# Performance work log

Measured on AMD Instinct MI355X. Metric: run time of the kernel, lower is better.

The kernel has to match this reference:

```python
import jax, jax.numpy as jnp
import numpy as np

DIM = 256
N = 8192

def setup_inputs() -> dict:
    key = jax.random.key(0)
    kx, kq, kk, kv = jax.random.split(key, 4)
    X = jax.random.normal(kx, (N, DIM), dtype=jnp.float32)
    # nn.Linear weights are [out, in]; xavier-uniform-like scale via normal/sqrt(dim)
    Wq = jax.random.normal(kq, (DIM, DIM), dtype=jnp.float32) / np.sqrt(DIM)
    Wk = jax.random.normal(kk, (DIM, DIM), dtype=jnp.float32) / np.sqrt(DIM)
    Wv = jax.random.normal(kv, (DIM, DIM), dtype=jnp.float32) / np.sqrt(DIM)
    return {"X": X, "Wq": Wq, "Wk": Wk, "Wv": Wv}

def reference(X, Wq, Wk, Wv):
    # nn.Linear(no bias): y = X @ W.T
    Q = X @ Wq.T  # [N, D]
    K = X @ Wk.T
    V = X @ Wv.T
    scores = (Q @ K.T) / jnp.sqrt(jnp.asarray(DIM, dtype=X.dtype))  # [N, N]
    softed = jax.nn.softmax(scores, axis=-1)
    return softed @ V  # [N, D]
```

## Files before the change

kernel.cpp:

```cpp
#include <hip/hip_runtime.h>
#include <math.h>

#define N 8192
#define D 256
#define QBLK 128
#define KBLK 32

typedef float f32x4 __attribute__((ext_vector_type(4)));
typedef float f32x16 __attribute__((ext_vector_type(16)));
typedef short bf16x8 __attribute__((ext_vector_type(8)));

#define MFMA16(a, b, c) __builtin_amdgcn_mfma_f32_16x16x32_bf16((a), (b), (c), 0, 0, 0)
#define MFMA32(a, b, c) __builtin_amdgcn_mfma_f32_32x32x16_bf16((a), (b), (c), 0, 0, 0)
#define BAR() __builtin_amdgcn_s_barrier()
#define CFENCE() asm volatile("" ::: "memory")

__device__ __forceinline__ unsigned short f2b(float f) {
    unsigned u = __builtin_bit_cast(unsigned, f);
    u = u + 0x7fffu + ((u >> 16) & 1u);
    return (unsigned short)(u >> 16);
}
__device__ __forceinline__ unsigned pk2(float a, float b) {
    return (unsigned)f2b(a) | ((unsigned)f2b(b) << 16);
}
__device__ __forceinline__ unsigned cvtpk(float a, float b) {
    unsigned r;
    asm("v_cvt_pk_bf16_f32 %0, %1, %2" : "=v"(r) : "v"(a), "v"(b));
    return r;
}
__device__ __forceinline__ float b2f(short s) {
    unsigned x = ((unsigned)(unsigned short)s) << 16;
    return __builtin_bit_cast(float, x);
}

__global__ __launch_bounds__(256) void proj_mfma(
    const float* __restrict__ X, const float* __restrict__ Wq,
    const float* __restrict__ Wk, const float* __restrict__ Wv,
    unsigned short* __restrict__ Qb, unsigned short* __restrict__ Kb,
    unsigned short* __restrict__ Vt)
{
    __shared__ char Wl[32768];
    const int z = blockIdx.z;
    const float* W = (z == 0) ? Wq : (z == 1) ? Wk : Wv;
    const int r0 = blockIdx.x * 64;
    const int c0 = blockIdx.y * 64;
    const int t = threadIdx.x, w = t >> 6, l = t & 63;
    const int lo = l & 15, hi = l >> 4;

    #pragma unroll
    for (int i = 0; i < 16; ++i) {
        int e4 = t + i * 256;
        int col = e4 >> 6, kk4 = e4 & 63;
        float4 f = *(const float4*)&W[(size_t)(c0 + col) * D + kk4 * 4];
        unsigned long long v = (unsigned long long)pk2(f.x, f.y)
                             | ((unsigned long long)pk2(f.z, f.w) << 32);
        *(unsigned long long*)(Wl + col * 512 + ((kk4 * 8) ^ ((col & 7) << 4))) = v;
    }
    __syncthreads();

    bf16x8 xf[8];
    {
        const float* xr = X + (size_t)(r0 + w * 16 + lo) * D;
        #pragma unroll
        for (int ks = 0; ks < 8; ++ks) {
            float4 a = *(const float4*)(xr + ks * 32 + hi * 8);
            float4 b = *(const float4*)(xr + ks * 32 + hi * 8 + 4);
            bf16x8 v;
            v[0] = (short)f2b(a.x); v[1] = (short)f2b(a.y);
            v[2] = (short)f2b(a.z); v[3] = (short)f2b(a.w);
            v[4] = (short)f2b(b.x); v[5] = (short)f2b(b.y);
            v[6] = (short)f2b(b.z); v[7] = (short)f2b(b.w);
            xf[ks] = v;
        }
    }

    f32x4 acc[4];
    #pragma unroll
    for (int nc = 0; nc < 4; ++nc) acc[nc] = (f32x4){0.f, 0.f, 0.f, 0.f};
    #pragma unroll
    for (int ks = 0; ks < 8; ++ks) {
        #pragma unroll
        for (int nc = 0; nc < 4; ++nc) {
            int col = nc * 16 + lo;
            bf16x8 wf = *(const bf16x8*)(Wl + col * 512 +
                                         ((ks * 64 + hi * 16) ^ ((col & 7) << 4)));
            acc[nc] = MFMA16(xf[ks], wf, acc[nc]);
        }
    }

    if (z < 2) {
        unsigned short* Y = z ? Kb : Qb;
        #pragma unroll
        for (int nc = 0; nc < 4; ++nc)
            #pragma unroll
            for (int r = 0; r < 4; ++r)
                Y[(size_t)(r0 + w * 16 + hi * 4 + r) * D + c0 + nc * 16 + lo] = f2b(acc[nc][r]);
    } else {
        #pragma unroll
        for (int nc = 0; nc < 4; ++nc) {
            unsigned long long v = (unsigned long long)pk2(acc[nc][0], acc[nc][1])
                                 | ((unsigned long long)pk2(acc[nc][2], acc[nc][3]) << 32);
            *(unsigned long long*)&Vt[(size_t)(c0 + nc * 16 + lo) * N + r0 + w * 16 + hi * 4] = v;
        }
    }
}

template <int KSPLIT>
__global__ __launch_bounds__(256, 2) void attn_mfma(
    const unsigned short* __restrict__ Qb,
    const unsigned short* __restrict__ Kb,
    const unsigned short* __restrict__ Vt,
    unsigned short* __restrict__ Opart,
    float2* __restrict__ ml)
{
    extern __shared__ char smem[];
    const int t = threadIdx.x;
    const int w = t >> 6;
    const int l = t & 63;
    const int r = l & 31;
    const int hi1 = l >> 5;
    const int bid = blockIdx.x;
    const int split = bid % KSPLIT;
    const int xblk = bid / KSPLIT;
    const int q0 = xblk * QBLK + w * 32;
    const int kbase = split * (N / KSPLIT);
    const int NTS = N / KSPLIT / KBLK;
    const int p0 = bid & (NTS - 1);

    unsigned ksoff[4], vsoff[4];
    #pragma unroll
    for (int i = 0; i < 4; ++i) {
        int c = t + i * 256;
        int rr = c >> 5, xc = c & 31;
        int pk = (rr & 0x13) | ((rr & 4) << 1) | ((rr & 8) >> 1);
        ksoff[i] = (unsigned)(pk * D + (xc ^ (rr & 7)) * 8);
        int dd = c >> 2, x2 = c & 3;
        vsoff[i] = (unsigned)(dd * N + (x2 ^ ((dd >> 1) & 3)) * 8);
    }

    auto stageK = [&](char* kbuf, int tile) {
        const unsigned koff = (unsigned)(kbase + tile * KBLK) * D;
        #pragma unroll
        for (int i = 0; i < 4; ++i)
            __builtin_amdgcn_global_load_lds(
                (const __attribute__((address_space(1))) void*)(Kb + koff + ksoff[i]),
                (__attribute__((address_space(3))) void*)(kbuf + (t + i * 256) * 16), 16, 0, 0);
    };
    auto stageV = [&](char* vbuf, int tile) {
        const unsigned voff = (unsigned)(kbase + tile * KBLK);
        #pragma unroll
        for (int i = 0; i < 4; ++i)
            __builtin_amdgcn_global_load_lds(
                (const __attribute__((address_space(1))) void*)(Vt + voff + vsoff[i]),
                (__attribute__((address_space(3))) void*)(vbuf + (t + i * 256) * 16), 16, 0, 0);
    };

    bf16x8 qf[16];
    {
        const unsigned short* qrow = Qb + (size_t)(q0 + r) * D;
        #pragma unroll
        for (int ks = 0; ks < 16; ++ks)
            qf[ks] = *(const bf16x8*)(qrow + ks * 16 + hi1 * 8);
    }

    stageK(smem, p0);
    stageV(smem + 32768, p0);
    stageK(smem + 16384, (p0 + 1) & (NTS - 1));
    stageV(smem + 32768 + 16384, (p0 + 1) & (NTS - 1));

    f32x16 Oacc[8];
    #pragma unroll
    for (int nc = 0; nc < 8; ++nc)
        #pragma unroll
        for (int e = 0; e < 16; ++e) Oacc[nc][e] = 0.f;
    float m_run = -INFINITY, l_run = 0.f;
    const float scale2 = 0.09016994f;

    for (int tt = 0; tt < NTS; ++tt) {
        const int cur = tt & 1;
        char* Kl = smem + cur * 16384;
        char* Vl = smem + 32768 + cur * 16384;

        if (tt + 1 == NTS) asm volatile("s_waitcnt vmcnt(0)" ::: "memory");
        else               asm volatile("s_waitcnt vmcnt(8)" ::: "memory");
        BAR(); CFENCE();

        f32x16 sacc;
        #pragma unroll
        for (int e = 0; e < 16; ++e) sacc[e] = 0.f;

        bf16x8 kf8[8];
        #pragma unroll
        for (int j = 0; j < 8; ++j)
            kf8[j] = *(const bf16x8*)(Kl + r * 512 + (((j * 2 + hi1) ^ (r & 7)) * 16));
        __builtin_amdgcn_s_setprio(1);
        #pragma unroll
        for (int j = 0; j < 8; ++j)
            sacc = MFMA32(kf8[j], qf[j], sacc);
        __builtin_amdgcn_s_setprio(0);

        bf16x8 kg8[8];
        #pragma unroll
        for (int j = 0; j < 8; ++j)
            kg8[j] = *(const bf16x8*)(Kl + r * 512 + ((((8 + j) * 2 + hi1) ^ (r & 7)) * 16));
        __builtin_amdgcn_s_setprio(1);
        #pragma unroll
        for (int j = 0; j < 8; ++j)
            sacc = MFMA32(kg8[j], qf[8 + j], sacc);
        __builtin_amdgcn_s_setprio(0);

        float m0 = fmaxf(fmaxf(sacc[0], sacc[1]),   fmaxf(sacc[2], sacc[3]));
        float m1 = fmaxf(fmaxf(sacc[4], sacc[5]),   fmaxf(sacc[6], sacc[7]));
        float m2 = fmaxf(fmaxf(sacc[8], sacc[9]),   fmaxf(sacc[10], sacc[11]));
        float m3 = fmaxf(fmaxf(sacc[12], sacc[13]), fmaxf(sacc[14], sacc[15]));
        float pm = fmaxf(fmaxf(m0, m1), fmaxf(m2, m3)) * scale2;

        bool need = pm > m_run + 11.0f;
        if (__builtin_expect(__any(need), 0)) {
            float m2x = fmaxf(pm, __shfl_xor(pm, 32));
            float m_new = fmaxf(m_run, m2x);
            float corr = exp2f(m_run - m_new);
            m_run = m_new;
            l_run *= corr;
            #pragma unroll
            for (int nc = 0; nc < 8; ++nc)
                #pragma unroll
                for (int e = 0; e < 16; ++e) Oacc[nc][e] *= corr;
        }

        bf16x8 pb[2];
        float sum = 0.f;
        #pragma unroll
        for (int s1 = 0; s1 < 2; ++s1) {
            union { unsigned u[4]; bf16x8 v; } uu;
            #pragma unroll
            for (int j2 = 0; j2 < 4; ++j2) {
                float a = __builtin_amdgcn_exp2f(sacc[s1 * 8 + j2 * 2]     * scale2 - m_run);
                float b = __builtin_amdgcn_exp2f(sacc[s1 * 8 + j2 * 2 + 1] * scale2 - m_run);
                sum += a + b;
                uu.u[j2] = cvtpk(a, b);
            }
            pb[s1] = uu.v;
        }

        bf16x8 vf8[8];
        #pragma unroll
        for (int nc = 0; nc < 4; ++nc) {
            const char* vrow = Vl + (nc * 32 + r) * 64;
            vf8[nc * 2 + 0] = *(const bf16x8*)(vrow + (((0 + hi1) ^ ((r >> 1) & 3)) * 16));
            vf8[nc * 2 + 1] = *(const bf16x8*)(vrow + (((2 + hi1) ^ ((r >> 1) & 3)) * 16));
        }
        __builtin_amdgcn_s_setprio(1);
        #pragma unroll
        for (int nc = 0; nc < 4; ++nc) {
            Oacc[nc] = MFMA32(vf8[nc * 2 + 0], pb[0], Oacc[nc]);
            Oacc[nc] = MFMA32(vf8[nc * 2 + 1], pb[1], Oacc[nc]);
        }
        __builtin_amdgcn_s_setprio(0);

        bf16x8 vg8[8];
        #pragma unroll
        for (int nc = 0; nc < 4; ++nc) {
            const char* vrow = Vl + ((nc + 4) * 32 + r) * 64;
            vg8[nc * 2 + 0] = *(const bf16x8*)(vrow + (((0 + hi1) ^ ((r >> 1) & 3)) * 16));
            vg8[nc * 2 + 1] = *(const bf16x8*)(vrow + (((2 + hi1) ^ ((r >> 1) & 3)) * 16));
        }
        __builtin_amdgcn_s_setprio(1);
        #pragma unroll
        for (int nc = 0; nc < 4; ++nc) {
            Oacc[nc + 4] = MFMA32(vg8[nc * 2 + 0], pb[0], Oacc[nc + 4]);
            Oacc[nc + 4] = MFMA32(vg8[nc * 2 + 1], pb[1], Oacc[nc + 4]);
        }
        __builtin_amdgcn_s_setprio(0);

        l_run += sum;

        CFENCE(); BAR(); CFENCE();
        if (tt + 2 < NTS) {
            const int nxt = (p0 + tt + 2) & (NTS - 1);
            stageK(Kl, nxt);
            stageV(Vl, nxt);
        }
    }

    l_run += __shfl_xor(l_run, 32);
    const size_t orow = ((size_t)split * N + q0 + r) * D;
    #pragma unroll
    for (int nc = 0; nc < 8; ++nc)
        #pragma unroll
        for (int g = 0; g < 4; ++g) {
            unsigned long long v =
                  (unsigned long long)pk2(Oacc[nc][g * 4 + 0], Oacc[nc][g * 4 + 1])
                | ((unsigned long long)pk2(Oacc[nc][g * 4 + 2], Oacc[nc][g * 4 + 3]) << 32);
            *(unsigned long long*)&Opart[orow + nc * 32 + g * 8 + hi1 * 4] = v;
        }
    if (l < 32)
        ml[(size_t)split * N + q0 + r] = make_float2(m_run, l_run);
}

__global__ __launch_bounds__(256) void combine_kernel(
    const unsigned short* __restrict__ Opart, const float2* __restrict__ ml,
    float* __restrict__ out, int nsplit)
{
    int idx = blockIdx.x * 256 + threadIdx.x;
    int q = idx >> 5;
    int d0 = (idx & 31) * 8;

    float M = -INFINITY;
    for (int i = 0; i < nsplit; ++i) M = fmaxf(M, ml[(size_t)i * N + q].x);
    float L = 0.f;
    float acc[8] = {};
    for (int i = 0; i < nsplit; ++i) {
        float2 v = ml[(size_t)i * N + q];
        float wgt = exp2f(v.x - M);
        L += wgt * v.y;
        bf16x8 ov = *(const bf16x8*)&Opart[((size_t)i * N + q) * D + d0];
        #pragma unroll
        for (int j = 0; j < 8; ++j) acc[j] += wgt * b2f(ov[j]);
    }
    float r = 1.f / L;
    #pragma unroll
    for (int j = 0; j < 8; ++j) out[(size_t)q * D + d0 + j] = acc[j] * r;
}

extern "C" void kernel_launch(void* const* d_in, const int* in_sizes, int n_in,
                              void* d_out, int out_size, void* d_ws, size_t ws_size,
                              hipStream_t stream) {
    const float* X  = (const float*)d_in[0];
    const float* Wq = (const float*)d_in[1];
    const float* Wk = (const float*)d_in[2];
    const float* Wv = (const float*)d_in[3];

    unsigned short* ws = (unsigned short*)d_ws;
    const size_t ndq = (size_t)N * D;
    unsigned short* Qb = ws;
    unsigned short* Kb = ws + ndq;
    unsigned short* Vt = ws + 2 * ndq;
    unsigned short* Opart = ws + 3 * ndq;

    auto need = [ndq](int ks) {
        return (size_t)(3 + ks) * ndq * 2 + (size_t)ks * N * 8;
    };
    const int ksplit = (ws_size >= need(8)) ? 8 : (ws_size >= need(4)) ? 4 : 2;
    float2* ml = (float2*)(ws + (3 + ksplit) * ndq);

    (void)hipFuncSetAttribute((const void*)attn_mfma<8>,
                              hipFuncAttributeMaxDynamicSharedMemorySize, 65536);
    (void)hipFuncSetAttribute((const void*)attn_mfma<4>,
                              hipFuncAttributeMaxDynamicSharedMemorySize, 65536);
    (void)hipFuncSetAttribute((const void*)attn_mfma<2>,
                              hipFuncAttributeMaxDynamicSharedMemorySize, 65536);

    proj_mfma<<<dim3(N / 64, D / 64, 3), 256, 0, stream>>>(X, Wq, Wk, Wv, Qb, Kb, Vt);
    if (ksplit == 8)
        attn_mfma<8><<<dim3((N / QBLK) * 8), 256, 65536, stream>>>(Qb, Kb, Vt, Opart, ml);
    else if (ksplit == 4)
        attn_mfma<4><<<dim3((N / QBLK) * 4), 256, 65536, stream>>>(Qb, Kb, Vt, Opart, ml);
    else
        attn_mfma<2><<<dim3((N / QBLK) * 2), 256, 65536, stream>>>(Qb, Kb, Vt, Opart, ml);
    combine_kernel<<<(N * D / 8) / 256, 256, 0, stream>>>(Opart, ml, (float*)d_out, ksplit);
}
```

Baseline: 125.9 us.

## Store V in MFMA fragment order and load it directly from global memory

The projection kernel now writes V in a fragment-ordered layout, so each lane's bf16x8 operand for the PV MFMA sits contiguously per key tile. The attention kernel drops V staging through LDS and loads V fragments straight from global/L2 into registers, issued before the softmax so the latency overlaps with that work. This halves LDS use and removes V barriers and LDS traffic. The cost is that every wave fetches V separately from global memory instead of sharing one LDS copy, which multiplies L2 traffic, and the vmcnt accounting now mixes direct loads with K staging.

```diff
diff --git a/kernel.cpp b/kernel.cpp
--- a/kernel.cpp
+++ b/kernel.cpp
@@ -37,7 +37,7 @@
     const float* __restrict__ X, const float* __restrict__ Wq,
     const float* __restrict__ Wk, const float* __restrict__ Wv,
     unsigned short* __restrict__ Qb, unsigned short* __restrict__ Kb,
-    unsigned short* __restrict__ Vt)
+    unsigned short* __restrict__ Vf)
 {
     __shared__ char Wl[32768];
     const int z = blockIdx.z;
@@ -96,11 +96,17 @@
             for (int r = 0; r < 4; ++r)
                 Y[(size_t)(r0 + w * 16 + hi * 4 + r) * D + c0 + nc * 16 + lo] = f2b(acc[nc][r]);
     } else {
+        const int keyb = r0 + w * 16 + hi * 4;
+        const int tile = keyb >> 5, kr = keyb & 31;
+        const int step = kr >> 4, h1v = (kr >> 3) & 1, jb = kr & 7;
         #pragma unroll
         for (int nc = 0; nc < 4; ++nc) {
+            int d = c0 + nc * 16 + lo;
+            int ncv = d >> 5, dr = d & 31;
             unsigned long long v = (unsigned long long)pk2(acc[nc][0], acc[nc][1])
                                  | ((unsigned long long)pk2(acc[nc][2], acc[nc][3]) << 32);
-            *(unsigned long long*)&Vt[(size_t)(c0 + nc * 16 + lo) * N + r0 + w * 16 + hi * 4] = v;
+            *(unsigned long long*)&Vf[(size_t)tile * 8192 + (ncv * 2 + step) * 512
+                                      + (h1v * 32 + dr) * 8 + jb] = v;
         }
     }
 }
@@ -109,7 +115,7 @@
 __global__ __launch_bounds__(256, 2) void attn_mfma(
     const unsigned short* __restrict__ Qb,
     const unsigned short* __restrict__ Kb,
-    const unsigned short* __restrict__ Vt,
+    const unsigned short* __restrict__ Vf,
     unsigned short* __restrict__ Opart,
     float2* __restrict__ ml)
 {
@@ -127,15 +133,13 @@
     const int NTS = N / KSPLIT / KBLK;
     const int p0 = bid & (NTS - 1);
 
-    unsigned ksoff[4], vsoff[4];
+    unsigned ksoff[4];
     #pragma unroll
     for (int i = 0; i < 4; ++i) {
         int c = t + i * 256;
         int rr = c >> 5, xc = c & 31;
         int pk = (rr & 0x13) | ((rr & 4) << 1) | ((rr & 8) >> 1);
         ksoff[i] = (unsigned)(pk * D + (xc ^ (rr & 7)) * 8);
-        int dd = c >> 2, x2 = c & 3;
-        vsoff[i] = (unsigned)(dd * N + (x2 ^ ((dd >> 1) & 3)) * 8);
     }
 
     auto stageK = [&](char* kbuf, int tile) {
@@ -146,14 +150,6 @@
                 (const __attribute__((address_space(1))) void*)(Kb + koff + ksoff[i]),
                 (__attribute__((address_space(3))) void*)(kbuf + (t + i * 256) * 16), 16, 0, 0);
     };
-    auto stageV = [&](char* vbuf, int tile) {
-        const unsigned voff = (unsigned)(kbase + tile * KBLK);
-        #pragma unroll
-        for (int i = 0; i < 4; ++i)
-            __builtin_amdgcn_global_load_lds(
-                (const __attribute__((address_space(1))) void*)(Vt + voff + vsoff[i]),
-                (__attribute__((address_space(3))) void*)(vbuf + (t + i * 256) * 16), 16, 0, 0);
-    };
 
     bf16x8 qf[16];
     {
@@ -163,10 +159,10 @@
             qf[ks] = *(const bf16x8*)(qrow + ks * 16 + hi1 * 8);
     }
 
+    const unsigned short* Vfl = Vf + (size_t)l * 8;
+
     stageK(smem, p0);
-    stageV(smem + 32768, p0);
     stageK(smem + 16384, (p0 + 1) & (NTS - 1));
-    stageV(smem + 32768 + 16384, (p0 + 1) & (NTS - 1));
 
     f32x16 Oacc[8];
     #pragma unroll
@@ -179,10 +175,11 @@
     for (int tt = 0; tt < NTS; ++tt) {
         const int cur = tt & 1;
         char* Kl = smem + cur * 16384;
-        char* Vl = smem + 32768 + cur * 16384;
+        const int tile = (p0 + tt) & (NTS - 1);
+        const size_t voff = ((size_t)(kbase / KBLK) + tile) * 8192;
 
         if (tt + 1 == NTS) asm volatile("s_waitcnt vmcnt(0)" ::: "memory");
-        else               asm volatile("s_waitcnt vmcnt(8)" ::: "memory");
+        else               asm volatile("s_waitcnt vmcnt(4)" ::: "memory");
         BAR(); CFENCE();
 
         f32x16 sacc;
@@ -208,6 +205,11 @@
         for (int j = 0; j < 8; ++j)
             sacc = MFMA32(kg8[j], qf[8 + j], sacc);
         __builtin_amdgcn_s_setprio(0);
+
+        bf16x8 vf8[8];
+        #pragma unroll
+        for (int c = 0; c < 8; ++c)
+            vf8[c] = *(const bf16x8*)(Vfl + voff + c * 512);
 
         float m0 = fmaxf(fmaxf(sacc[0], sacc[1]),   fmaxf(sacc[2], sacc[3]));
         float m1 = fmaxf(fmaxf(sacc[4], sacc[5]),   fmaxf(sacc[6], sacc[7]));
@@ -243,13 +245,6 @@
             pb[s1] = uu.v;
         }
 
-        bf16x8 vf8[8];
-        #pragma unroll
-        for (int nc = 0; nc < 4; ++nc) {
-            const char* vrow = Vl + (nc * 32 + r) * 64;
-            vf8[nc * 2 + 0] = *(const bf16x8*)(vrow + (((0 + hi1) ^ ((r >> 1) & 3)) * 16));
-            vf8[nc * 2 + 1] = *(const bf16x8*)(vrow + (((2 + hi1) ^ ((r >> 1) & 3)) * 16));
-        }
         __builtin_amdgcn_s_setprio(1);
         #pragma unroll
         for (int nc = 0; nc < 4; ++nc) {
@@ -260,11 +255,8 @@
 
         bf16x8 vg8[8];
         #pragma unroll
-        for (int nc = 0; nc < 4; ++nc) {
-            const char* vrow = Vl + ((nc + 4) * 32 + r) * 64;
-            vg8[nc * 2 + 0] = *(const bf16x8*)(vrow + (((0 + hi1) ^ ((r >> 1) & 3)) * 16));
-            vg8[nc * 2 + 1] = *(const bf16x8*)(vrow + (((2 + hi1) ^ ((r >> 1) & 3)) * 16));
-        }
+        for (int c = 0; c < 8; ++c)
+            vg8[c] = *(const bf16x8*)(Vfl + voff + (8 + c) * 512);
         __builtin_amdgcn_s_setprio(1);
         #pragma unroll
         for (int nc = 0; nc < 4; ++nc) {
@@ -276,11 +268,8 @@
         l_run += sum;
 
         CFENCE(); BAR(); CFENCE();
-        if (tt + 2 < NTS) {
-            const int nxt = (p0 + tt + 2) & (NTS - 1);
-            stageK(Kl, nxt);
-            stageV(Vl, nxt);
-        }
+        if (tt + 2 < NTS)
+            stageK(Kl, (p0 + tt + 2) & (NTS - 1));
     }
 
     l_run += __shfl_xor(l_run, 32);
@@ -335,7 +324,7 @@
     const size_t ndq = (size_t)N * D;
     unsigned short* Qb = ws;
     unsigned short* Kb = ws + ndq;
-    unsigned short* Vt = ws + 2 * ndq;
+    unsigned short* Vf = ws + 2 * ndq;
     unsigned short* Opart = ws + 3 * ndq;
 
     auto need = [ndq](int ks) {
@@ -345,18 +334,18 @@
     float2* ml = (float2*)(ws + (3 + ksplit) * ndq);
 
     (void)hipFuncSetAttribute((const void*)attn_mfma<8>,
-                              hipFuncAttributeMaxDynamicSharedMemorySize, 65536);
+                              hipFuncAttributeMaxDynamicSharedMemorySize, 32768);
     (void)hipFuncSetAttribute((const void*)attn_mfma<4>,
-                              hipFuncAttributeMaxDynamicSharedMemorySize, 65536);
+                              hipFuncAttributeMaxDynamicSharedMemorySize, 32768);
     (void)hipFuncSetAttribute((const void*)attn_mfma<2>,
-                              hipFuncAttributeMaxDynamicSharedMemorySize, 65536);
-
-    proj_mfma<<<dim3(N / 64, D / 64, 3), 256, 0, stream>>>(X, Wq, Wk, Wv, Qb, Kb, Vt);
+                              hipFuncAttributeMaxDynamicSharedMemorySize, 32768);
+
+    proj_mfma<<<dim3(N / 64, D / 64, 3), 256, 0, stream>>>(X, Wq, Wk, Wv, Qb, Kb, Vf);
     if (ksplit == 8)
-        attn_mfma<8><<<dim3((N / QBLK) * 8), 256, 65536, stream>>>(Qb, Kb, Vt, Opart, ml);
+        attn_mfma<8><<<dim3((N / QBLK) * 8), 256, 32768, stream>>>(Qb, Kb, Vf, Opart, ml);
     else if (ksplit == 4)
-        attn_mfma<4><<<dim3((N / QBLK) * 4), 256, 65536, stream>>>(Qb, Kb, Vt, Opart, ml);
+        attn_mfma<4><<<dim3((N / QBLK) * 4), 256, 32768, stream>>>(Qb, Kb, Vf, Opart, ml);
     else
-        attn_mfma<2><<<dim3((N / QBLK) * 2), 256, 65536, stream>>>(Qb, Kb, Vt, Opart, ml);
+        attn_mfma<2><<<dim3((N / QBLK) * 2), 256, 32768, stream>>>(Qb, Kb, Vf, Opart, ml);
     combine_kernel<<<(N * D / 8) / 256, 256, 0, stream>>>(Opart, ml, (float*)d_out, ksplit);
 }
```

Measured after the change: 135.7 us. 7.8% more time.

## Double attention block size to 512 threads and use triple-buffered K/V staging

Applied to the files above, without the earlier changes.

The attention kernel now runs 8 waves over 256 query rows per block, so each K/V tile loaded into LDS is shared by twice as many query rows. The K/V prefetch moves from double to triple buffering: the next-next tile is issued at the top of each iteration, before the barrier, rather than after compute. This lowers global and LDS staging traffic per query and overlaps loads with compute more deeply. The costs are 96KB of LDS per block and half as many blocks, which may lower occupancy and leave parallelism thin across the CUs.

```diff
diff --git a/kernel.cpp b/kernel.cpp
--- a/kernel.cpp
+++ b/kernel.cpp
@@ -3,7 +3,7 @@
 
 #define N 8192
 #define D 256
-#define QBLK 128
+#define QBLK 256
 #define KBLK 32
 
 typedef float f32x4 __attribute__((ext_vector_type(4)));
@@ -106,7 +106,7 @@
 }
 
 template <int KSPLIT>
-__global__ __launch_bounds__(256, 2) void attn_mfma(
+__global__ __launch_bounds__(512, 2) void attn_mfma(
     const unsigned short* __restrict__ Qb,
     const unsigned short* __restrict__ Kb,
     const unsigned short* __restrict__ Vt,
@@ -125,12 +125,12 @@
     const int q0 = xblk * QBLK + w * 32;
     const int kbase = split * (N / KSPLIT);
     const int NTS = N / KSPLIT / KBLK;
-    const int p0 = bid & (NTS - 1);
-
-    unsigned ksoff[4], vsoff[4];
-    #pragma unroll
-    for (int i = 0; i < 4; ++i) {
-        int c = t + i * 256;
+    const int p0 = xblk & (NTS - 1);
+
+    unsigned ksoff[2], vsoff[2];
+    #pragma unroll
+    for (int i = 0; i < 2; ++i) {
+        int c = t + i * 512;
         int rr = c >> 5, xc = c & 31;
         int pk = (rr & 0x13) | ((rr & 4) << 1) | ((rr & 8) >> 1);
         ksoff[i] = (unsigned)(pk * D + (xc ^ (rr & 7)) * 8);
@@ -138,21 +138,19 @@
         vsoff[i] = (unsigned)(dd * N + (x2 ^ ((dd >> 1) & 3)) * 8);
     }
 
-    auto stageK = [&](char* kbuf, int tile) {
-        const unsigned koff = (unsigned)(kbase + tile * KBLK) * D;
-        #pragma unroll
-        for (int i = 0; i < 4; ++i)
+    auto stage = [&](char* buf, int tile) {
+        const unsigned kv0 = (unsigned)(kbase + tile * KBLK);
+        const unsigned koff = kv0 * D;
+        #pragma unroll
+        for (int i = 0; i < 2; ++i)
             __builtin_amdgcn_global_load_lds(
                 (const __attribute__((address_space(1))) void*)(Kb + koff + ksoff[i]),
-                (__attribute__((address_space(3))) void*)(kbuf + (t + i * 256) * 16), 16, 0, 0);
-    };
-    auto stageV = [&](char* vbuf, int tile) {
-        const unsigned voff = (unsigned)(kbase + tile * KBLK);
-        #pragma unroll
-        for (int i = 0; i < 4; ++i)
+                (__attribute__((address_space(3))) void*)(buf + (t + i * 512) * 16), 16, 0, 0);
+        #pragma unroll
+        for (int i = 0; i < 2; ++i)
             __builtin_amdgcn_global_load_lds(
-                (const __attribute__((address_space(1))) void*)(Vt + voff + vsoff[i]),
-                (__attribute__((address_space(3))) void*)(vbuf + (t + i * 256) * 16), 16, 0, 0);
+                (const __attribute__((address_space(1))) void*)(Vt + kv0 + vsoff[i]),
+                (__attribute__((address_space(3))) void*)(buf + 16384 + (t + i * 512) * 16), 16, 0, 0);
     };
 
     bf16x8 qf[16];
@@ -163,10 +161,8 @@
             qf[ks] = *(const bf16x8*)(qrow + ks * 16 + hi1 * 8);
     }
 
-    stageK(smem, p0);
-    stageV(smem + 32768, p0);
-    stageK(smem + 16384, (p0 + 1) & (NTS - 1));
-    stageV(smem + 32768 + 16384, (p0 + 1) & (NTS - 1));
+    stage(smem, p0);
+    stage(smem + 32768, (p0 + 1) & (NTS - 1));
 
     f32x16 Oacc[8];
     #pragma unroll
@@ -176,13 +172,20 @@
     float m_run = -INFINITY, l_run = 0.f;
     const float scale2 = 0.09016994f;
 
+    int bcur = 0;
     for (int tt = 0; tt < NTS; ++tt) {
-        const int cur = tt & 1;
-        char* Kl = smem + cur * 16384;
-        char* Vl = smem + 32768 + cur * 16384;
-
-        if (tt + 1 == NTS) asm volatile("s_waitcnt vmcnt(0)" ::: "memory");
-        else               asm volatile("s_waitcnt vmcnt(8)" ::: "memory");
+        char* Kl = smem + bcur * 32768;
+        char* Vl = Kl + 16384;
+
+        if (tt + 2 < NTS) {
+            int bnx = bcur + 2; if (bnx >= 3) bnx -= 3;
+            stage(smem + bnx * 32768, (p0 + tt + 2) & (NTS - 1));
+            asm volatile("s_waitcnt vmcnt(8)" ::: "memory");
+        } else if (tt + 1 < NTS) {
+            asm volatile("s_waitcnt vmcnt(4)" ::: "memory");
+        } else {
+            asm volatile("s_waitcnt vmcnt(0)" ::: "memory");
+        }
         BAR(); CFENCE();
 
         f32x16 sacc;
@@ -276,11 +279,7 @@
         l_run += sum;
 
         CFENCE(); BAR(); CFENCE();
-        if (tt + 2 < NTS) {
-            const int nxt = (p0 + tt + 2) & (NTS - 1);
-            stageK(Kl, nxt);
-            stageV(Vl, nxt);
-        }
+        ++bcur; if (bcur == 3) bcur = 0;
     }
 
     l_run += __shfl_xor(l_run, 32);
@@ -345,18 +344,18 @@
     float2* ml = (float2*)(ws + (3 + ksplit) * ndq);
 
     (void)hipFuncSetAttribute((const void*)attn_mfma<8>,
-                              hipFuncAttributeMaxDynamicSharedMemorySize, 65536);
+                              hipFuncAttributeMaxDynamicSharedMemorySize, 98304);
     (void)hipFuncSetAttribute((const void*)attn_mfma<4>,
-                              hipFuncAttributeMaxDynamicSharedMemorySize, 65536);
+                              hipFuncAttributeMaxDynamicSharedMemorySize, 98304);
     (void)hipFuncSetAttribute((const void*)attn_mfma<2>,
-                              hipFuncAttributeMaxDynamicSharedMemorySize, 65536);
+                              hipFuncAttributeMaxDynamicSharedMemorySize, 98304);
 
     proj_mfma<<<dim3(N / 64, D / 64, 3), 256, 0, stream>>>(X, Wq, Wk, Wv, Qb, Kb, Vt);
     if (ksplit == 8)
-        attn_mfma<8><<<dim3((N / QBLK) * 8), 256, 65536, stream>>>(Qb, Kb, Vt, Opart, ml);
+        attn_mfma<8><<<dim3((N / QBLK) * 8), 512, 98304, stream>>>(Qb, Kb, Vt, Opart, ml);
     else if (ksplit == 4)
-        attn_mfma<4><<<dim3((N / QBLK) * 4), 256, 65536, stream>>>(Qb, Kb, Vt, Opart, ml);
+        attn_mfma<4><<<dim3((N / QBLK) * 4), 512, 98304, stream>>>(Qb, Kb, Vt, Opart, ml);
     else
-        attn_mfma<2><<<dim3((N / QBLK) * 2), 256, 65536, stream>>>(Qb, Kb, Vt, Opart, ml);
+        attn_mfma<2><<<dim3((N / QBLK) * 2), 512, 98304, stream>>>(Qb, Kb, Vt, Opart, ml);
     combine_kernel<<<(N * D / 8) / 256, 256, 0, stream>>>(Opart, ml, (float*)d_out, ksplit);
 }
```

After: 123.0 us. 2.3% less time.
